# Performance work log

Measured on AMD Instinct MI355X. Metric: run time of the kernel, lower is better.

Reference implementation:

```python
import jax, jax.numpy as jnp
import numpy as np


def setup_inputs() -> dict:
    key = jax.random.key(0)
    k1, k2, k3, k4 = jax.random.split(key, 4)
    Q, K, D, H = 8, 1024, 64, 1024
    B, T = 8, 8192
    codes = jax.random.randint(k1, (Q, B, T), 0, K, dtype=jnp.int64)
    codebooks = jax.random.normal(k2, (Q, K, D), dtype=jnp.float32)
    W = jax.random.normal(k3, (Q, H, D), dtype=jnp.float32)  # nn.Linear weight layout [out, in]
    b = jax.random.normal(k4, (Q, H), dtype=jnp.float32)
    return {"codes": codes, "codebooks": codebooks, "W": W, "b": b}


def reference(codes, codebooks, W, b):
    # codes: [Q, B, T] int; codebooks: [Q, K, D]; W: [Q, H, D]; b: [Q, H]
    # gather per-quantizer codebook entries -> [Q, B, T, D]
    emb = jax.vmap(lambda cb, c: cb[c])(codebooks, codes)
    # project to hidden and sum over quantizers -> [B, H, T] (matches permute(0,2,1))
    out = jnp.einsum("qbtd,qhd->bht", emb, W)
    # bias is added per quantizer, then summed -> sum of biases broadcast over B, T
    out = out + jnp.sum(b, axis=0)[None, :, None]
    return out
```

## Files before the change

kernel.cpp:

```cpp
#include <hip/hip_runtime.h>
#include <hip/hip_bf16.h>

#define NQ 8
#define NK 1024
#define ND 64
#define NH 1024
#define NB 8
#define NT 8192

typedef float  vfloat4 __attribute__((ext_vector_type(4)));
typedef float  vfloat2 __attribute__((ext_vector_type(2)));
typedef float  f32x4   __attribute__((ext_vector_type(4)));
typedef short  short8  __attribute__((ext_vector_type(8)));

__device__ __forceinline__ unsigned cvt_pk_bf16(float lo, float hi) {
    unsigned r;
    asm("v_cvt_pk_bf16_f32 %0, %1, %2" : "=v"(r) : "v"(lo), "v"(hi));
    return r;
}

__global__ __launch_bounds__(256) void to_bf16(const float* __restrict__ cb,
                                               const float* __restrict__ W,
                                               uint4* __restrict__ cbh,
                                               uint4* __restrict__ Wh) {
    int half = blockIdx.x >> 8;
    int i    = ((blockIdx.x & 255) << 8) + threadIdx.x;
    const float4* src = (const float4*)(half ? W : cb);
    float4 a = src[i * 2], b = src[i * 2 + 1];
    uint4 o;
    o.x = cvt_pk_bf16(a.x, a.y);
    o.y = cvt_pk_bf16(a.z, a.w);
    o.z = cvt_pk_bf16(b.x, b.y);
    o.w = cvt_pk_bf16(b.z, b.w);
    (half ? Wh : cbh)[i] = o;
}

__global__ __launch_bounds__(256) void build_Pt(const short* __restrict__ cbh,
                                                const short* __restrict__ Wh,
                                                const float* __restrict__ bias,
                                                uint2* __restrict__ Pt) {
    int q    = blockIdx.x >> 8;
    int rest = blockIdx.x & 255;
    int hb   = rest >> 4;
    int kb   = rest & 15;
    int wave = threadIdx.x >> 6, lane = threadIdx.x & 63;
    int h_tile = hb * 64 + wave * 16;
    int row16 = lane & 15, grp = lane >> 4;

    short8 afrag[2];
    const short* wrow = Wh + ((size_t)q * NH + h_tile + row16) * ND + grp * 8;
    afrag[0] = *(const short8*)(wrow);
    afrag[1] = *(const short8*)(wrow + 32);

    float bvals[4];
#pragma unroll
    for (int r = 0; r < 4; ++r) bvals[r] = bias[q * NH + h_tile + grp * 4 + r];

    int k0 = kb * 64;
    const short* cbase = cbh + ((size_t)q * NK + k0 + row16) * ND + grp * 8;
    int hg = (h_tile >> 2) + grp;

#pragma unroll
    for (int t = 0; t < 4; ++t) {
        const short* crow = cbase + (size_t)t * 16 * ND;
        short8 b0 = *(const short8*)(crow);
        short8 b1 = *(const short8*)(crow + 32);
        f32x4 acc = {0.f, 0.f, 0.f, 0.f};
        acc = __builtin_amdgcn_mfma_f32_16x16x32_bf16(afrag[0], b0, acc, 0, 0, 0);
        acc = __builtin_amdgcn_mfma_f32_16x16x32_bf16(afrag[1], b1, acc, 0, 0, 0);
        int k = k0 + t * 16 + row16;
        uint2 pk;
        pk.x = cvt_pk_bf16(acc[0] + bvals[0], acc[1] + bvals[1]);
        pk.y = cvt_pk_bf16(acc[2] + bvals[2], acc[3] + bvals[3]);
        Pt[((size_t)hg * NQ + q) * NK + k] = pk;
    }
}

__global__ __launch_bounds__(512, 4) void gather_sum(const int* __restrict__ codes,
                                                     const uint2* __restrict__ Pt,
                                                     float* __restrict__ out) {
    int b   = blockIdx.x & 7;
    int hg  = blockIdx.x >> 3;
    int tid = threadIdx.x;

    __shared__ uint2 Pl[NQ * NK];
    const uint4* src = (const uint4*)(Pt + (size_t)hg * NQ * NK);
    uint4* dst = (uint4*)Pl;
#pragma unroll
    for (int i = 0; i < 8; ++i) dst[tid + i * 512] = src[tid + i * 512];
    __syncthreads();

    int h0 = hg * 4;
    for (int j = 0; j < 4; ++j) {
        int t0 = j * 2048 + tid * 4;
        vfloat2 acc[4][2];
#pragma unroll
        for (int tt = 0; tt < 4; ++tt) {
            acc[tt][0] = (vfloat2){0.f, 0.f};
            acc[tt][1] = (vfloat2){0.f, 0.f};
        }

#pragma unroll
        for (int q = 0; q < NQ; ++q) {
            int4 cc = *(const int4*)(codes + ((size_t)q * NB + b) * NT + t0);
#pragma unroll
            for (int tt = 0; tt < 4; ++tt) {
                int c = (tt == 0) ? cc.x : (tt == 1) ? cc.y : (tt == 2) ? cc.z : cc.w;
                uint2 v = Pl[q * NK + c];
                vfloat2 a0 = {__uint_as_float(v.x << 16), __uint_as_float(v.x)};
                vfloat2 a1 = {__uint_as_float(v.y << 16), __uint_as_float(v.y)};
                acc[tt][0] += a0;
                acc[tt][1] += a1;
            }
        }
#pragma unroll
        for (int hh = 0; hh < 4; ++hh) {
            vfloat4 o;
            o[0] = acc[0][hh >> 1][hh & 1];
            o[1] = acc[1][hh >> 1][hh & 1];
            o[2] = acc[2][hh >> 1][hh & 1];
            o[3] = acc[3][hh >> 1][hh & 1];
            vfloat4* dstp = (vfloat4*)(out + ((size_t)b * NH + (h0 + hh)) * NT + t0);
            __builtin_nontemporal_store(o, dstp);
        }
    }
}

extern "C" void kernel_launch(void* const* d_in, const int* in_sizes, int n_in,
                              void* d_out, int out_size, void* d_ws, size_t ws_size,
                              hipStream_t stream) {
    const int*   codes = (const int*)d_in[0];
    const float* cb    = (const float*)d_in[1];
    const float* W     = (const float*)d_in[2];
    const float* bias  = (const float*)d_in[3];
    float*       out   = (float*)d_out;

    uint2* Pt  = (uint2*)d_ws;
    uint4* cbh = (uint4*)((char*)d_ws + (16u << 20));
    uint4* Wh  = (uint4*)((char*)d_ws + (17u << 20));

    to_bf16<<<512, 256, 0, stream>>>(cb, W, cbh, Wh);
    build_Pt<<<2048, 256, 0, stream>>>((const short*)cbh, (const short*)Wh, bias, Pt);
    gather_sum<<<256 * NB, 512, 0, stream>>>(codes, Pt, out);
}
```

Baseline: 85.55 us.

## Fuse projection-table build into gather kernel and add summed bias in fp32

Drops the separate build_Pt kernel and its global Pt table. Each block of the new fused kernel computes its own 4-row slice of the codebook-times-W table with MFMA straight into shared memory, then gathers and sums over all batches for half of T. Bias is now summed across quantizers and added in fp32 at output time instead of being folded into each bf16 table entry. The gain is one fewer launch and no table round-trip through global memory. The cost is redundant MFMA work (each block computes 16 rows but keeps 4), a serial 64-iteration global-load loop per wave, and a grid cut to 512 larger blocks.

```diff
diff --git a/kernel.cpp b/kernel.cpp
--- a/kernel.cpp
+++ b/kernel.cpp
@@ -18,6 +18,10 @@
     asm("v_cvt_pk_bf16_f32 %0, %1, %2" : "=v"(r) : "v"(lo), "v"(hi));
     return r;
 }
+__device__ __forceinline__ unsigned bf16_rne(float f) {
+    unsigned u = __float_as_uint(f);
+    return (u + 0x7fffu + ((u >> 16) & 1u)) >> 16;
+}
 
 __global__ __launch_bounds__(256) void to_bf16(const float* __restrict__ cb,
                                                const float* __restrict__ W,
@@ -35,71 +39,68 @@
     (half ? Wh : cbh)[i] = o;
 }
 
-__global__ __launch_bounds__(256) void build_Pt(const short* __restrict__ cbh,
-                                                const short* __restrict__ Wh,
-                                                const float* __restrict__ bias,
-                                                uint2* __restrict__ Pt) {
-    int q    = blockIdx.x >> 8;
-    int rest = blockIdx.x & 255;
-    int hb   = rest >> 4;
-    int kb   = rest & 15;
-    int wave = threadIdx.x >> 6, lane = threadIdx.x & 63;
-    int h_tile = hb * 64 + wave * 16;
+__global__ __launch_bounds__(512) void fused_rvq(const int* __restrict__ codes,
+                                                 const short* __restrict__ cbh,
+                                                 const short* __restrict__ Wh,
+                                                 const float* __restrict__ bias,
+                                                 float* __restrict__ out) {
+    __shared__ uint2 Pl[NQ * NK];
+
+    int hb = blockIdx.x >> 1;
+    int th = blockIdx.x & 1;
+    int h0 = hb * 4;
+    int tid  = threadIdx.x;
+    int wave = tid >> 6, lane = tid & 63;
     int row16 = lane & 15, grp = lane >> 4;
 
-    short8 afrag[2];
-    const short* wrow = Wh + ((size_t)q * NH + h_tile + row16) * ND + grp * 8;
-    afrag[0] = *(const short8*)(wrow);
-    afrag[1] = *(const short8*)(wrow + 32);
-
-    float bvals[4];
+    uint2 z; z.x = 0u; z.y = 0u;
 #pragma unroll
-    for (int r = 0; r < 4; ++r) bvals[r] = bias[q * NH + h_tile + grp * 4 + r];
-
-    int k0 = kb * 64;
-    const short* cbase = cbh + ((size_t)q * NK + k0 + row16) * ND + grp * 8;
-    int hg = (h_tile >> 2) + grp;
-
-#pragma unroll
-    for (int t = 0; t < 4; ++t) {
-        const short* crow = cbase + (size_t)t * 16 * ND;
-        short8 b0 = *(const short8*)(crow);
-        short8 b1 = *(const short8*)(crow + 32);
-        f32x4 acc = {0.f, 0.f, 0.f, 0.f};
-        acc = __builtin_amdgcn_mfma_f32_16x16x32_bf16(afrag[0], b0, acc, 0, 0, 0);
-        acc = __builtin_amdgcn_mfma_f32_16x16x32_bf16(afrag[1], b1, acc, 0, 0, 0);
-        int k = k0 + t * 16 + row16;
-        uint2 pk;
-        pk.x = cvt_pk_bf16(acc[0] + bvals[0], acc[1] + bvals[1]);
-        pk.y = cvt_pk_bf16(acc[2] + bvals[2], acc[3] + bvals[3]);
-        Pt[((size_t)hg * NQ + q) * NK + k] = pk;
-    }
-}
-
-__global__ __launch_bounds__(512, 4) void gather_sum(const int* __restrict__ codes,
-                                                     const uint2* __restrict__ Pt,
-                                                     float* __restrict__ out) {
-    int b   = blockIdx.x & 7;
-    int hg  = blockIdx.x >> 3;
-    int tid = threadIdx.x;
-
-    __shared__ uint2 Pl[NQ * NK];
-    const uint4* src = (const uint4*)(Pt + (size_t)hg * NQ * NK);
-    uint4* dst = (uint4*)Pl;
-#pragma unroll
-    for (int i = 0; i < 8; ++i) dst[tid + i * 512] = src[tid + i * 512];
+    for (int i = 0; i < 16; ++i) Pl[tid + i * 512] = z;
     __syncthreads();
 
-    int h0 = hg * 4;
-    for (int j = 0; j < 4; ++j) {
-        int t0 = j * 2048 + tid * 4;
+    {
+        int q = wave;
+        int hrow = h0 + row16;
+        if (hrow > NH - 1) hrow = NH - 1;
+        const short* wrow = Wh + ((size_t)q * NH + hrow) * ND + grp * 8;
+        short8 a0 = *(const short8*)(wrow);
+        short8 a1 = *(const short8*)(wrow + 32);
+        for (int kt = 0; kt < 64; ++kt) {
+            const short* crow = cbh + ((size_t)q * NK + kt * 16 + row16) * ND + grp * 8;
+            short8 b0 = *(const short8*)(crow);
+            short8 b1 = *(const short8*)(crow + 32);
+            f32x4 acc = {0.f, 0.f, 0.f, 0.f};
+            acc = __builtin_amdgcn_mfma_f32_16x16x32_bf16(a0, b0, acc, 0, 0, 0);
+            acc = __builtin_amdgcn_mfma_f32_16x16x32_bf16(a1, b1, acc, 0, 0, 0);
+            unsigned px = bf16_rne(acc[0]) | (bf16_rne(acc[1]) << 16);
+            unsigned py = bf16_rne(acc[2]) | (bf16_rne(acc[3]) << 16);
+            if (grp == 0) {
+                uint2 pk; pk.x = px; pk.y = py;
+                Pl[q * NK + kt * 16 + row16] = pk;
+            }
+        }
+    }
+
+    float bsum[4];
+#pragma unroll
+    for (int hh = 0; hh < 4; ++hh) {
+        float s = 0.f;
+#pragma unroll
+        for (int q = 0; q < NQ; ++q) s += bias[q * NH + h0 + hh];
+        bsum[hh] = s;
+    }
+    __syncthreads();
+
+#pragma unroll 1
+    for (int jj = 0; jj < 16; ++jj) {
+        int b  = jj >> 1;
+        int t0 = th * (NT / 2) + (jj & 1) * 2048 + tid * 4;
         vfloat2 acc[4][2];
 #pragma unroll
         for (int tt = 0; tt < 4; ++tt) {
             acc[tt][0] = (vfloat2){0.f, 0.f};
             acc[tt][1] = (vfloat2){0.f, 0.f};
         }
-
 #pragma unroll
         for (int q = 0; q < NQ; ++q) {
             int4 cc = *(const int4*)(codes + ((size_t)q * NB + b) * NT + t0);
@@ -107,19 +108,17 @@
             for (int tt = 0; tt < 4; ++tt) {
                 int c = (tt == 0) ? cc.x : (tt == 1) ? cc.y : (tt == 2) ? cc.z : cc.w;
                 uint2 v = Pl[q * NK + c];
-                vfloat2 a0 = {__uint_as_float(v.x << 16), __uint_as_float(v.x)};
-                vfloat2 a1 = {__uint_as_float(v.y << 16), __uint_as_float(v.y)};
-                acc[tt][0] += a0;
-                acc[tt][1] += a1;
+                acc[tt][0] += (vfloat2){__uint_as_float(v.x << 16), __uint_as_float(v.x)};
+                acc[tt][1] += (vfloat2){__uint_as_float(v.y << 16), __uint_as_float(v.y)};
             }
         }
 #pragma unroll
         for (int hh = 0; hh < 4; ++hh) {
             vfloat4 o;
-            o[0] = acc[0][hh >> 1][hh & 1];
-            o[1] = acc[1][hh >> 1][hh & 1];
-            o[2] = acc[2][hh >> 1][hh & 1];
-            o[3] = acc[3][hh >> 1][hh & 1];
+            o[0] = acc[0][hh >> 1][hh & 1] + bsum[hh];
+            o[1] = acc[1][hh >> 1][hh & 1] + bsum[hh];
+            o[2] = acc[2][hh >> 1][hh & 1] + bsum[hh];
+            o[3] = acc[3][hh >> 1][hh & 1] + bsum[hh];
             vfloat4* dstp = (vfloat4*)(out + ((size_t)b * NH + (h0 + hh)) * NT + t0);
             __builtin_nontemporal_store(o, dstp);
         }
@@ -135,11 +134,10 @@
     const float* bias  = (const float*)d_in[3];
     float*       out   = (float*)d_out;
 
-    uint2* Pt  = (uint2*)d_ws;
     uint4* cbh = (uint4*)((char*)d_ws + (16u << 20));
     uint4* Wh  = (uint4*)((char*)d_ws + (17u << 20));
 
     to_bf16<<<512, 256, 0, stream>>>(cb, W, cbh, Wh);
-    build_Pt<<<2048, 256, 0, stream>>>((const short*)cbh, (const short*)Wh, bias, Pt);
-    gather_sum<<<256 * NB, 512, 0, stream>>>(codes, Pt, out);
+    fused_rvq<<<512, 512, 0, stream>>>(codes, (const short*)cbh, (const short*)Wh,
+                                       bias, out);
 }
```

Result: slower. 109.2 us (+27.7%).

## Interleave projection table pairs and gather 8 hidden rows per LDS read

Applied to the files above, without the earlier changes.

build_Pt now writes the projected table so that two adjacent 4-row hidden groups sit interleaved. Each 16-byte LDS read in the gather kernel therefore yields 8 hidden values instead of 4. The gather kernel becomes one 1024-thread block per 8 hidden rows and half of T, looping over all batches. This halves code-index reads and LDS lookups per output, and the table is staged once per block rather than once per batch. In exchange each block uses 128KB of LDS, which limits the GPU to one block per CU with 256 blocks total, and there is less latency hiding and no overlap of the table load with compute.

```diff
diff --git a/kernel.cpp b/kernel.cpp
--- a/kernel.cpp
+++ b/kernel.cpp
@@ -38,7 +38,7 @@
 __global__ __launch_bounds__(256) void build_Pt(const short* __restrict__ cbh,
                                                 const short* __restrict__ Wh,
                                                 const float* __restrict__ bias,
-                                                uint2* __restrict__ Pt) {
+                                                uint2* __restrict__ Pt2) {
     int q    = blockIdx.x >> 8;
     int rest = blockIdx.x & 255;
     int hb   = rest >> 4;
@@ -72,33 +72,33 @@
         uint2 pk;
         pk.x = cvt_pk_bf16(acc[0] + bvals[0], acc[1] + bvals[1]);
         pk.y = cvt_pk_bf16(acc[2] + bvals[2], acc[3] + bvals[3]);
-        Pt[((size_t)hg * NQ + q) * NK + k] = pk;
+        Pt2[((((size_t)(hg >> 1) * NQ) + q) * NK + k) * 2 + (hg & 1)] = pk;
     }
 }
 
-__global__ __launch_bounds__(512, 4) void gather_sum(const int* __restrict__ codes,
-                                                     const uint2* __restrict__ Pt,
-                                                     float* __restrict__ out) {
-    int b   = blockIdx.x & 7;
-    int hg  = blockIdx.x >> 3;
+__global__ __launch_bounds__(1024) void gather_sum8(const int* __restrict__ codes,
+                                                    const uint4* __restrict__ Pt4,
+                                                    float* __restrict__ out) {
+    int th  = blockIdx.x & 1;
+    int hg8 = blockIdx.x >> 1;
     int tid = threadIdx.x;
 
-    __shared__ uint2 Pl[NQ * NK];
-    const uint4* src = (const uint4*)(Pt + (size_t)hg * NQ * NK);
-    uint4* dst = (uint4*)Pl;
+    __shared__ uint4 Pl[NQ * NK];
+    const uint4* src = Pt4 + (size_t)hg8 * NQ * NK;
 #pragma unroll
-    for (int i = 0; i < 8; ++i) dst[tid + i * 512] = src[tid + i * 512];
+    for (int i = 0; i < 8; ++i) Pl[tid + i * 1024] = src[tid + i * 1024];
     __syncthreads();
 
-    int h0 = hg * 4;
-    for (int j = 0; j < 4; ++j) {
-        int t0 = j * 2048 + tid * 4;
-        vfloat2 acc[4][2];
+    int h0 = hg8 * 8;
+    int t0 = th * (NT / 2) + tid * 4;
+
+#pragma unroll 1
+    for (int b = 0; b < NB; ++b) {
+        vfloat2 acc[4][4];
 #pragma unroll
-        for (int tt = 0; tt < 4; ++tt) {
-            acc[tt][0] = (vfloat2){0.f, 0.f};
-            acc[tt][1] = (vfloat2){0.f, 0.f};
-        }
+        for (int tt = 0; tt < 4; ++tt)
+#pragma unroll
+            for (int p = 0; p < 4; ++p) acc[tt][p] = (vfloat2){0.f, 0.f};
 
 #pragma unroll
         for (int q = 0; q < NQ; ++q) {
@@ -106,15 +106,15 @@
 #pragma unroll
             for (int tt = 0; tt < 4; ++tt) {
                 int c = (tt == 0) ? cc.x : (tt == 1) ? cc.y : (tt == 2) ? cc.z : cc.w;
-                uint2 v = Pl[q * NK + c];
-                vfloat2 a0 = {__uint_as_float(v.x << 16), __uint_as_float(v.x)};
-                vfloat2 a1 = {__uint_as_float(v.y << 16), __uint_as_float(v.y)};
-                acc[tt][0] += a0;
-                acc[tt][1] += a1;
+                uint4 v = Pl[q * NK + c];
+                acc[tt][0] += (vfloat2){__uint_as_float(v.x << 16), __uint_as_float(v.x)};
+                acc[tt][1] += (vfloat2){__uint_as_float(v.y << 16), __uint_as_float(v.y)};
+                acc[tt][2] += (vfloat2){__uint_as_float(v.z << 16), __uint_as_float(v.z)};
+                acc[tt][3] += (vfloat2){__uint_as_float(v.w << 16), __uint_as_float(v.w)};
             }
         }
 #pragma unroll
-        for (int hh = 0; hh < 4; ++hh) {
+        for (int hh = 0; hh < 8; ++hh) {
             vfloat4 o;
             o[0] = acc[0][hh >> 1][hh & 1];
             o[1] = acc[1][hh >> 1][hh & 1];
@@ -135,11 +135,11 @@
     const float* bias  = (const float*)d_in[3];
     float*       out   = (float*)d_out;
 
-    uint2* Pt  = (uint2*)d_ws;
+    uint2* Pt2 = (uint2*)d_ws;
     uint4* cbh = (uint4*)((char*)d_ws + (16u << 20));
     uint4* Wh  = (uint4*)((char*)d_ws + (17u << 20));
 
     to_bf16<<<512, 256, 0, stream>>>(cb, W, cbh, Wh);
-    build_Pt<<<2048, 256, 0, stream>>>((const short*)cbh, (const short*)Wh, bias, Pt);
-    gather_sum<<<256 * NB, 512, 0, stream>>>(codes, Pt, out);
+    build_Pt<<<2048, 256, 0, stream>>>((const short*)cbh, (const short*)Wh, bias, Pt2);
+    gather_sum8<<<256, 1024, 0, stream>>>(codes, (const uint4*)Pt2, out);
 }
```

Measured after the change: 74.19 us, median of 2. 13.3% less time.
